# Performance work log

Hardware: AMD Instinct MI355X
Metric: run time of the kernel (lower is better)

The kernel has to match this reference:

```python
import jax, jax.numpy as jnp
import numpy as np

DIM, HEADS, HDIM, B, L = 2048, 16, 128, 2, 2048

def setup_inputs() -> dict:
    key = jax.random.key(0)
    ks = jax.random.split(key, 7)
    s = 1.0 / np.sqrt(DIM)
    return {
        "x": jax.random.normal(ks[0], (B, L, DIM), jnp.float32),
        "rope_emb": jax.random.uniform(ks[1], (L, HDIM), jnp.float32),
        "wq": jax.random.normal(ks[2], (DIM, DIM), jnp.float32) * s,
        "wk": jax.random.normal(ks[3], (DIM, DIM), jnp.float32) * s,
        "wv": jax.random.normal(ks[4], (DIM, DIM), jnp.float32) * s,
        "wo": jax.random.normal(ks[5], (DIM, DIM), jnp.float32) * s,
        "bo": jnp.zeros((DIM,), jnp.float32),
    }

def _rotate_half(x):
    x1, x2 = jnp.split(x, 2, axis=-1)
    return jnp.concatenate((-x2, x1), axis=-1)

def reference(x, rope_emb, wq, wk, wv, wo, bo):
    Bq, Lq, D = x.shape
    # projections; torch Linear: y = x @ W.T, weights here stored as [out,in]
    q = jnp.einsum("bld,ed->ble", x, wq).reshape(Bq, Lq, HEADS, HDIM).transpose(0, 2, 1, 3)
    k = jnp.einsum("bld,ed->ble", x, wk).reshape(Bq, Lq, HEADS, HDIM).transpose(0, 2, 1, 3)
    v = jnp.einsum("bld,ed->ble", x, wv).reshape(Bq, Lq, HEADS, HDIM).transpose(0, 2, 1, 3)
    cos = jnp.cos(rope_emb)[None, None]  # [1,1,L,hd]
    sin = jnp.sin(rope_emb)[None, None]
    q = q * cos + _rotate_half(q) * sin
    k = k * cos + _rotate_half(k) * sin
    scale = HDIM ** -0.5
    attn = jnp.einsum("bhqd,bhkd->bhqk", q, k) * scale
    attn = jax.nn.softmax(attn, axis=-1)
    out = jnp.einsum("bhqk,bhkd->bhqd", attn, v)
    out = out.transpose(0, 2, 1, 3).reshape(Bq, Lq, D)
    return jnp.einsum("bld,ed->ble", out, wo) + bo
```

## Files before the change

### kernel.cpp

```cpp
#include <hip/hip_runtime.h>
#include <hip/hip_bf16.h>
#include <stdint.h>

#define DIMS  2048
#define HEADS 16
#define HD    128
#define BATCH 2
#define SEQ   2048
#define MROWS (BATCH*SEQ)
#define QKVN  (3*DIMS)

using bf16x8 = __attribute__((ext_vector_type(8))) short;
using f32x4  = __attribute__((ext_vector_type(4))) float;
using f32x16 = __attribute__((ext_vector_type(16))) float;
using u16x4  = __attribute__((ext_vector_type(4))) unsigned short;

__device__ __forceinline__ unsigned short f2b(float f){
    __hip_bfloat16 h = __float2bfloat16(f);
    return *reinterpret_cast<unsigned short*>(&h);
}
__device__ __forceinline__ float b2f(unsigned short u){
    __hip_bfloat16 h;
    *reinterpret_cast<unsigned short*>(&h) = u;
    return __bfloat162float(h);
}
__device__ __forceinline__ unsigned int pkbf(float lo, float hi){
    return (unsigned int)f2b(lo) | ((unsigned int)f2b(hi) << 16);
}

__device__ __forceinline__ void glds16(const void* g, void* l){
    __builtin_amdgcn_global_load_lds(
        (const __attribute__((address_space(1))) unsigned int*)g,
        (__attribute__((address_space(3))) unsigned int*)l, 16, 0, 0);
}


__global__ void k_f32bf16(const float* __restrict__ src, unsigned short* __restrict__ dst, int n4){
    int i = blockIdx.x*blockDim.x + threadIdx.x;
    if (i >= n4) return;
    const float4 v = reinterpret_cast<const float4*>(src)[i];
    u16x4 o = { f2b(v.x), f2b(v.y), f2b(v.z), f2b(v.w) };
    *reinterpret_cast<u16x4*>(dst + 4*(size_t)i) = o;
}

__global__ void k_wconv4(const float* __restrict__ w0, const float* __restrict__ w1,
                         const float* __restrict__ w2, const float* __restrict__ w3,
                         unsigned short* __restrict__ d0, unsigned short* __restrict__ d1,
                         unsigned short* __restrict__ d2, unsigned short* __restrict__ d3){
    const int sel = blockIdx.y;
    const float* src = sel==0 ? w0 : sel==1 ? w1 : sel==2 ? w2 : w3;
    unsigned short* dst = sel==0 ? d0 : sel==1 ? d1 : sel==2 ? d2 : d3;
    const int i = blockIdx.x*blockDim.x + threadIdx.x;
    const float4 v = reinterpret_cast<const float4*>(src)[i];
    u16x4 o = { f2b(v.x), f2b(v.y), f2b(v.z), f2b(v.w) };
    *reinterpret_cast<u16x4*>(dst + 4*(size_t)i) = o;
}

__global__ void k_cossin(const float* __restrict__ r, float* __restrict__ c, float* __restrict__ s, int n){
    int i = blockIdx.x*blockDim.x + threadIdx.x;
    if (i >= n) return;
    float v = r[i];
    c[i] = cosf(v);
    s[i] = sinf(v);
}

__global__ void k_rope(unsigned short* __restrict__ qkv,
                       const float* __restrict__ ct, const float* __restrict__ st){
    const int idx = blockIdx.x*blockDim.x + threadIdx.x;
    const int d0 = (idx & 7) << 3;
    const int h  = (idx >> 3) & (HEADS-1);
    const int l  = (idx >> 7) & (SEQ-1);
    const int b  = idx >> 18;

    const float4* cp = reinterpret_cast<const float4*>(ct + l*HD + d0);
    const float4* sp = reinterpret_cast<const float4*>(st + l*HD + d0);
    const float4 cl0 = cp[0],  cl1 = cp[1];
    const float4 sl0 = sp[0],  sl1 = sp[1];
    const float4 cu0 = cp[16], cu1 = cp[17];
    const float4 su0 = sp[16], su1 = sp[17];
    const float cl[8] = {cl0.x,cl0.y,cl0.z,cl0.w, cl1.x,cl1.y,cl1.z,cl1.w};
    const float sl[8] = {sl0.x,sl0.y,sl0.z,sl0.w, sl1.x,sl1.y,sl1.z,sl1.w};
    const float cu[8] = {cu0.x,cu0.y,cu0.z,cu0.w, cu1.x,cu1.y,cu1.z,cu1.w};
    const float su[8] = {su0.x,su0.y,su0.z,su0.w, su1.x,su1.y,su1.z,su1.w};

    unsigned short* base = qkv + (size_t)(b*SEQ + l)*QKVN + h*HD + d0;
    #pragma unroll
    for (int s = 0; s < 2; ++s){
        unsigned short* rp = base + s*DIMS;
        bf16x8 lo = *reinterpret_cast<const bf16x8*>(rp);
        bf16x8 hi = *reinterpret_cast<const bf16x8*>(rp + 64);
        bf16x8 olo, ohi;
        #pragma unroll
        for (int j = 0; j < 8; ++j){
            const float x1 = b2f((unsigned short)lo[j]);
            const float x2 = b2f((unsigned short)hi[j]);
            olo[j] = (short)f2b(x1*cl[j] - x2*sl[j]);
            ohi[j] = (short)f2b(x2*cu[j] + x1*su[j]);
        }
        *reinterpret_cast<bf16x8*>(rp)      = olo;
        *reinterpret_cast<bf16x8*>(rp + 64) = ohi;
    }
}

__global__ void k_vtrans(const unsigned short* __restrict__ qkv, unsigned short* __restrict__ vt){
    __shared__ unsigned short t[64*68];
    const int lt = blockIdx.x;
    const int dt = blockIdx.y;
    const int bh = blockIdx.z;
    const int b = bh >> 4, h = bh & 15;
    const int tid = threadIdx.x;
    const int l0 = lt << 6;
    #pragma unroll
    for (int it = 0; it < 4; ++it){
        const int c = tid + (it<<8);
        const int l = c >> 4;
        const int d4 = (c & 15) << 2;
        const u16x4 v = *reinterpret_cast<const u16x4*>(
            qkv + (size_t)(b*SEQ + l0 + l)*QKVN + 2*DIMS + h*HD + (dt<<6) + d4);
        *reinterpret_cast<u16x4*>(&t[l*68 + d4]) = v;
    }
    __syncthreads();
    #pragma unroll
    for (int it = 0; it < 4; ++it){
        const int c = tid + (it<<8);
        const int d = c >> 4;
        const int l4 = (c & 15) << 2;
        u16x4 o = { t[(l4+0)*68 + d], t[(l4+1)*68 + d], t[(l4+2)*68 + d], t[(l4+3)*68 + d] };
        *reinterpret_cast<u16x4*>(&vt[((size_t)bh*HD + (dt<<6) + d)*SEQ + l0 + l4]) = o;
    }
}


template<int FINAL>
__global__ __launch_bounds__(256) void k_gemm_bt(
    const unsigned short* __restrict__ A, const unsigned short* __restrict__ B,
    void* __restrict__ C, const float* __restrict__ bias, int M, int N, int K)
{
    __shared__ unsigned short lA[128*64];
    __shared__ unsigned short lB[128*64];
    const int tid  = threadIdx.x;
    const int lane = tid & 63;
    const int wave = tid >> 6;

    const int nbx = N >> 7;
    const int nwg = gridDim.x;
    const int cpx = nwg >> 3;
    const int bid = blockIdx.x;
    const int wg  = (bid & 7)*cpx + (bid >> 3);
    const int m0 = (wg / nbx) << 7;
    const int n0 = (wg % nbx) << 7;

    const int wr = (wave >> 1) << 6;
    const int wc = (wave & 1) << 6;

    f32x4 acc[4][4] = {};

    const int srow_base = (wave<<3) + (lane>>3);
    const int schunk = lane & 7;

    for (int k0 = 0; k0 < K; k0 += 64){
        #pragma unroll
        for (int i = 0; i < 4; ++i){
            const int row  = (i<<5) + srow_base;
            const int scol = k0 + ((schunk ^ (row & 7)) << 3);
            glds16(A + (size_t)(m0 + row)*K + scol, &lA[((i<<5) + (wave<<3)) << 6]);
            glds16(B + (size_t)(n0 + row)*K + scol, &lB[((i<<5) + (wave<<3)) << 6]);
        }
        __syncthreads();
        #pragma unroll
        for (int ks = 0; ks < 2; ++ks){
            bf16x8 af[4], bfr[4];
            const int colbase = (ks<<5) + ((lane>>4)<<3);
            #pragma unroll
            for (int mi = 0; mi < 4; ++mi){
                const int row = wr + (mi<<4) + (lane & 15);
                af[mi] = *reinterpret_cast<const bf16x8*>(&lA[(row<<6) + (colbase ^ ((row&7)<<3))]);
            }
            #pragma unroll
            for (int ni = 0; ni < 4; ++ni){
                const int row = wc + (ni<<4) + (lane & 15);
                bfr[ni] = *reinterpret_cast<const bf16x8*>(&lB[(row<<6) + (colbase ^ ((row&7)<<3))]);
            }
            #pragma unroll
            for (int mi = 0; mi < 4; ++mi)
                #pragma unroll
                for (int ni = 0; ni < 4; ++ni)
                    acc[mi][ni] = __builtin_amdgcn_mfma_f32_16x16x32_bf16(af[mi], bfr[ni], acc[mi][ni], 0, 0, 0);
        }
        __syncthreads();
    }

    const int r0 = (lane >> 4) << 2;
    const int cn = lane & 15;
    #pragma unroll
    for (int mi = 0; mi < 4; ++mi)
        #pragma unroll
        for (int r = 0; r < 4; ++r){
            const int gm = m0 + wr + (mi<<4) + r0 + r;
            #pragma unroll
            for (int ni = 0; ni < 4; ++ni){
                const int gn = n0 + wc + (ni<<4) + cn;
                const float v = acc[mi][ni][r];
                if (FINAL)
                    reinterpret_cast<float*>(C)[(size_t)gm*N + gn] = v + bias[gn];
                else
                    reinterpret_cast<unsigned short*>(C)[(size_t)gm*N + gn] = f2b(v);
            }
        }
}


union U8 { unsigned int w[4]; bf16x8 v; };

__global__ __launch_bounds__(256, 2) void k_attn(
    const unsigned short* __restrict__ qkv, const unsigned short* __restrict__ vt,
    unsigned short* __restrict__ aout)
{
    __shared__ unsigned short smem[32768];

    const int tid  = threadIdx.x;
    const int lane = tid & 63;
    const int wave = tid >> 6;
    const int lq   = lane & 31;
    const int hi   = lane >> 5;
    const int bh = blockIdx.y;
    const int b = bh >> 4, h = bh & 15;
    const int q0w = (blockIdx.x << 7) + (wave << 5);

    const unsigned short* Kb = qkv + (size_t)b*SEQ*QKVN + DIMS + h*HD;
    const unsigned short* Vb = vt + (size_t)bh*HD*SEQ;

    bf16x8 qf[8];
    {
        const float qscale = 0.08838834764831845f * 1.4426950408889634f;
        const unsigned short* qp = qkv + (size_t)(b*SEQ + q0w + lq)*QKVN + h*HD + (hi<<3);
        #pragma unroll
        for (int ks = 0; ks < 8; ++ks){
            bf16x8 tv = *reinterpret_cast<const bf16x8*>(qp + (ks<<4));
            #pragma unroll
            for (int j = 0; j < 8; ++j)
                tv[j] = (short)f2b(b2f((unsigned short)tv[j]) * qscale);
            qf[ks] = tv;
        }
    }

    float m_run = -3e38f, l_run = 0.f;
    f32x16 oacc[4] = {};

    #define STAGE(pb, kv0) do { \
        _Pragma("unroll") \
        for (int i = 0; i < 4; ++i){ \
            const int kr = (wave<<4) + (i<<2) + (lane>>4); \
            glds16(Kb + (size_t)((kv0) + kr)*QKVN + (((lane&15) ^ (kr&7))<<3), \
                   &smem[((pb)<<13) + (((wave<<4) + (i<<2))<<7)]); \
            const int dr = (wave<<5) + (i<<3) + (lane>>3); \
            glds16(Vb + (size_t)dr*SEQ + (kv0) + (((lane&7) ^ (dr&7))<<3), \
                   &smem[16384 + ((pb)<<13) + (((wave<<5) + (i<<3))<<6)]); \
        } \
    } while(0)

    int buf = 0;
    STAGE(0, 0);
    __syncthreads();

    for (int t = 0; t < SEQ/64; ++t){
        if (t < SEQ/64 - 1) STAGE(buf^1, (t+1)*64);

        const unsigned short* Kbuf = &smem[buf<<13];
        const unsigned short* Vbuf = &smem[16384 + (buf<<13)];

        f32x16 st0 = {}, st1 = {};
        __builtin_amdgcn_s_setprio(1);
        #pragma unroll
        for (int ks = 0; ks < 8; ++ks){
            const int col = (((ks<<1) + hi) ^ (lq & 7)) << 3;
            bf16x8 k0 = *reinterpret_cast<const bf16x8*>(&Kbuf[(lq<<7) + col]);
            bf16x8 k1 = *reinterpret_cast<const bf16x8*>(&Kbuf[((32+lq)<<7) + col]);
            st0 = __builtin_amdgcn_mfma_f32_32x32x16_bf16(k0, qf[ks], st0, 0, 0, 0);
            st1 = __builtin_amdgcn_mfma_f32_32x32x16_bf16(k1, qf[ks], st1, 0, 0, 0);
        }
        __builtin_amdgcn_s_setprio(0);

        float tmax = st0[0];
        #pragma unroll
        for (int r = 1; r < 16; ++r) tmax = fmaxf(tmax, st0[r]);
        #pragma unroll
        for (int r = 0; r < 16; ++r) tmax = fmaxf(tmax, st1[r]);
        tmax = fmaxf(tmax, __shfl_xor(tmax, 32));

        const bool defer = __all(tmax <= m_run + 8.0f);
        if (!defer){
            const float mnew = fmaxf(m_run, tmax);
            const float al = __builtin_amdgcn_exp2f(m_run - mnew);
            m_run = mnew;
            l_run *= al;
            #pragma unroll
            for (int dt = 0; dt < 4; ++dt) oacc[dt] *= al;
        }
        float tsum = 0.f;
        #pragma unroll
        for (int r = 0; r < 16; ++r){ float p = __builtin_amdgcn_exp2f(st0[r] - m_run); st0[r] = p; tsum += p; }
        #pragma unroll
        for (int r = 0; r < 16; ++r){ float p = __builtin_amdgcn_exp2f(st1[r] - m_run); st1[r] = p; tsum += p; }
        tsum += __shfl_xor(tsum, 32);
        l_run += tsum;

        bf16x8 pf[4];
        #define MAKEPF(dA, dB, SV) do { \
            unsigned int a0 = pkbf(SV[0],SV[1]),  b0 = pkbf(SV[2],SV[3]); \
            unsigned int c0 = pkbf(SV[4],SV[5]),  d0 = pkbf(SV[6],SV[7]); \
            unsigned int a1 = pkbf(SV[8],SV[9]),  b1 = pkbf(SV[10],SV[11]); \
            unsigned int c1 = pkbf(SV[12],SV[13]),d1 = pkbf(SV[14],SV[15]); \
            asm("v_permlane32_swap_b32 %0, %1" : "+v"(a0), "+v"(c0)); \
            asm("v_permlane32_swap_b32 %0, %1" : "+v"(b0), "+v"(d0)); \
            asm("v_permlane32_swap_b32 %0, %1" : "+v"(a1), "+v"(c1)); \
            asm("v_permlane32_swap_b32 %0, %1" : "+v"(b1), "+v"(d1)); \
            U8 u; \
            u.w[0] = a0; u.w[1] = b0; u.w[2] = c0; u.w[3] = d0; dA = u.v; \
            u.w[0] = a1; u.w[1] = b1; u.w[2] = c1; u.w[3] = d1; dB = u.v; \
        } while(0)
        MAKEPF(pf[0], pf[1], st0);
        MAKEPF(pf[2], pf[3], st1);
        #undef MAKEPF

        __builtin_amdgcn_s_setprio(1);
        #pragma unroll
        for (int dt = 0; dt < 4; ++dt){
            const int rowv = (dt<<5) + lq;
            #pragma unroll
            for (int f = 0; f < 4; ++f){
                const int col = (((f<<1) + hi) ^ (lq & 7)) << 3;
                bf16x8 vf = *reinterpret_cast<const bf16x8*>(&Vbuf[(rowv<<6) + col]);
                oacc[dt] = __builtin_amdgcn_mfma_f32_32x32x16_bf16(vf, pf[f], oacc[dt], 0, 0, 0);
            }
        }
        __builtin_amdgcn_s_setprio(0);

        __syncthreads();
        buf ^= 1;
    }
    #undef STAGE

    const float rl = 1.0f / l_run;
    unsigned short* oL = smem + wave*(32*132);
    #pragma unroll
    for (int dt = 0; dt < 4; ++dt)
        #pragma unroll
        for (int g = 0; g < 4; ++g){
            u16x4 w = { f2b(oacc[dt][g*4+0]*rl), f2b(oacc[dt][g*4+1]*rl),
                        f2b(oacc[dt][g*4+2]*rl), f2b(oacc[dt][g*4+3]*rl) };
            *reinterpret_cast<u16x4*>(&oL[lq*132 + (dt<<5) + (hi<<2) + (g<<3)]) = w;
        }
    #pragma unroll
    for (int i = 0; i < 16; ++i){
        const int q = (i<<1) + hi;
        u16x4 w = *reinterpret_cast<const u16x4*>(&oL[q*132 + (lq<<2)]);
        *reinterpret_cast<u16x4*>(&aout[(size_t)(b*SEQ + q0w + q)*DIMS + h*HD + (lq<<2)]) = w;
    }
}


extern "C" void kernel_launch(void* const* d_in, const int* in_sizes, int n_in,
                              void* d_out, int out_size, void* d_ws, size_t ws_size,
                              hipStream_t stream)
{
    const float* x    = (const float*)d_in[0];
    const float* rope = (const float*)d_in[1];
    const float* wq   = (const float*)d_in[2];
    const float* wk   = (const float*)d_in[3];
    const float* wv   = (const float*)d_in[4];
    const float* wo   = (const float*)d_in[5];
    const float* bo   = (const float*)d_in[6];
    float* out = (float*)d_out;

    char* ws = (char*)d_ws;
    unsigned short* x_bf   = (unsigned short*)(ws + 0);
    unsigned short* wqkv   = (unsigned short*)(ws + 16777216);
    unsigned short* wo_bf  = (unsigned short*)(ws + 41943040);
    float*          cos_t  = (float*)(ws + 50331648);
    float*          sin_t  = (float*)(ws + 51380224);
    unsigned short* qkv    = (unsigned short*)(ws + 52428800);
    unsigned short* vt     = (unsigned short*)(ws + 16777216);
    unsigned short* a_out  = (unsigned short*)(ws + 0);

    k_f32bf16<<<8192, 256, 0, stream>>>(x, x_bf, 2097152);
    k_wconv4<<<dim3(4096,4), 256, 0, stream>>>(wq, wk, wv, wo,
                                               wqkv, wqkv + 4194304, wqkv + 8388608, wo_bf);
    k_cossin <<<1024, 256, 0, stream>>>(rope, cos_t, sin_t, SEQ*HD);

    k_gemm_bt<0><<<(MROWS/128)*(QKVN/128), 256, 0, stream>>>(x_bf, wqkv, qkv, nullptr, MROWS, QKVN, DIMS);

    k_rope<<<2048, 256, 0, stream>>>(qkv, cos_t, sin_t);

    k_vtrans<<<dim3(SEQ/64, HD/64, BATCH*HEADS), 256, 0, stream>>>(qkv, vt);

    k_attn<<<dim3(SEQ/128, BATCH*HEADS), 256, 0, stream>>>(qkv, vt, a_out);

    k_gemm_bt<1><<<(MROWS/128)*(DIMS/128), 256, 0, stream>>>(a_out, wo_bf, out, bo, MROWS, DIMS, DIMS);
}
```

Measured before the change: 287.5 us.

## Merge prep kernels, fuse K-rope with V transpose, apply Q-rope inside attention

Folds the x/weight bf16 conversions and the cos/sin table into one launch. K-rope and the V transpose now share a single kernel, which removes two launches and the separate Q-rope pass over global memory. Q rotary embedding is applied in registers while Q fragments are loaded in the attention kernel, combined with the softmax scale. The trade-off is extra cos/sin table loads and arithmetic in attention setup, plus a larger branchy prep grid.

```diff
diff --git a/kernel.cpp b/kernel.cpp
--- a/kernel.cpp
+++ b/kernel.cpp
@@ -35,58 +35,60 @@
 }
 
 
-__global__ void k_f32bf16(const float* __restrict__ src, unsigned short* __restrict__ dst, int n4){
-    int i = blockIdx.x*blockDim.x + threadIdx.x;
-    if (i >= n4) return;
+__global__ void k_prep(const float* __restrict__ x,
+                       const float* __restrict__ w0, const float* __restrict__ w1,
+                       const float* __restrict__ w2, const float* __restrict__ w3,
+                       const float* __restrict__ rope,
+                       unsigned short* __restrict__ x_bf,
+                       unsigned short* __restrict__ d0, unsigned short* __restrict__ d1,
+                       unsigned short* __restrict__ d2, unsigned short* __restrict__ d3,
+                       float* __restrict__ ct, float* __restrict__ st){
+    const int y = blockIdx.y;
+    if (y == 6){
+        const int i = blockIdx.x*blockDim.x + threadIdx.x;
+        if (i >= SEQ*HD) return;
+        const float v = rope[i];
+        ct[i] = cosf(v);
+        st[i] = sinf(v);
+        return;
+    }
+    const float* src;
+    unsigned short* dst;
+    size_t off = 0;
+    if      (y == 0){ src = w0; dst = d0; }
+    else if (y == 1){ src = w1; dst = d1; }
+    else if (y == 2){ src = w2; dst = d2; }
+    else if (y == 3){ src = w3; dst = d3; }
+    else            { src = x;  dst = x_bf; off = (size_t)(y - 4) * 1048576; }
+    const size_t i = off + blockIdx.x*blockDim.x + threadIdx.x;
     const float4 v = reinterpret_cast<const float4*>(src)[i];
     u16x4 o = { f2b(v.x), f2b(v.y), f2b(v.z), f2b(v.w) };
-    *reinterpret_cast<u16x4*>(dst + 4*(size_t)i) = o;
-}
-
-__global__ void k_wconv4(const float* __restrict__ w0, const float* __restrict__ w1,
-                         const float* __restrict__ w2, const float* __restrict__ w3,
-                         unsigned short* __restrict__ d0, unsigned short* __restrict__ d1,
-                         unsigned short* __restrict__ d2, unsigned short* __restrict__ d3){
-    const int sel = blockIdx.y;
-    const float* src = sel==0 ? w0 : sel==1 ? w1 : sel==2 ? w2 : w3;
-    unsigned short* dst = sel==0 ? d0 : sel==1 ? d1 : sel==2 ? d2 : d3;
-    const int i = blockIdx.x*blockDim.x + threadIdx.x;
-    const float4 v = reinterpret_cast<const float4*>(src)[i];
-    u16x4 o = { f2b(v.x), f2b(v.y), f2b(v.z), f2b(v.w) };
-    *reinterpret_cast<u16x4*>(dst + 4*(size_t)i) = o;
-}
-
-__global__ void k_cossin(const float* __restrict__ r, float* __restrict__ c, float* __restrict__ s, int n){
-    int i = blockIdx.x*blockDim.x + threadIdx.x;
-    if (i >= n) return;
-    float v = r[i];
-    c[i] = cosf(v);
-    s[i] = sinf(v);
-}
-
-__global__ void k_rope(unsigned short* __restrict__ qkv,
-                       const float* __restrict__ ct, const float* __restrict__ st){
-    const int idx = blockIdx.x*blockDim.x + threadIdx.x;
-    const int d0 = (idx & 7) << 3;
-    const int h  = (idx >> 3) & (HEADS-1);
-    const int l  = (idx >> 7) & (SEQ-1);
-    const int b  = idx >> 18;
-
-    const float4* cp = reinterpret_cast<const float4*>(ct + l*HD + d0);
-    const float4* sp = reinterpret_cast<const float4*>(st + l*HD + d0);
-    const float4 cl0 = cp[0],  cl1 = cp[1];
-    const float4 sl0 = sp[0],  sl1 = sp[1];
-    const float4 cu0 = cp[16], cu1 = cp[17];
-    const float4 su0 = sp[16], su1 = sp[17];
-    const float cl[8] = {cl0.x,cl0.y,cl0.z,cl0.w, cl1.x,cl1.y,cl1.z,cl1.w};
-    const float sl[8] = {sl0.x,sl0.y,sl0.z,sl0.w, sl1.x,sl1.y,sl1.z,sl1.w};
-    const float cu[8] = {cu0.x,cu0.y,cu0.z,cu0.w, cu1.x,cu1.y,cu1.z,cu1.w};
-    const float su[8] = {su0.x,su0.y,su0.z,su0.w, su1.x,su1.y,su1.z,su1.w};
-
-    unsigned short* base = qkv + (size_t)(b*SEQ + l)*QKVN + h*HD + d0;
-    #pragma unroll
-    for (int s = 0; s < 2; ++s){
-        unsigned short* rp = base + s*DIMS;
+    *reinterpret_cast<u16x4*>(dst + 4*i) = o;
+}
+
+
+__global__ void k_kropevt(unsigned short* __restrict__ qkv,
+                          const float* __restrict__ ct, const float* __restrict__ st,
+                          unsigned short* __restrict__ vt){
+    __shared__ unsigned short t[64*68];
+    const int bid = blockIdx.x;
+    if (bid < 2048){
+        const int idx = bid*blockDim.x + threadIdx.x;
+        const int d0 = (idx & 7) << 3;
+        const int h  = (idx >> 3) & (HEADS-1);
+        const int l  = (idx >> 7) & (SEQ-1);
+        const int b  = idx >> 18;
+        const float4* cp = reinterpret_cast<const float4*>(ct + l*HD + d0);
+        const float4* sp = reinterpret_cast<const float4*>(st + l*HD + d0);
+        const float4 cl0 = cp[0],  cl1 = cp[1];
+        const float4 sl0 = sp[0],  sl1 = sp[1];
+        const float4 cu0 = cp[16], cu1 = cp[17];
+        const float4 su0 = sp[16], su1 = sp[17];
+        const float cl[8] = {cl0.x,cl0.y,cl0.z,cl0.w, cl1.x,cl1.y,cl1.z,cl1.w};
+        const float sl[8] = {sl0.x,sl0.y,sl0.z,sl0.w, sl1.x,sl1.y,sl1.z,sl1.w};
+        const float cu[8] = {cu0.x,cu0.y,cu0.z,cu0.w, cu1.x,cu1.y,cu1.z,cu1.w};
+        const float su[8] = {su0.x,su0.y,su0.z,su0.w, su1.x,su1.y,su1.z,su1.w};
+        unsigned short* rp = qkv + (size_t)(b*SEQ + l)*QKVN + DIMS + h*HD + d0;
         bf16x8 lo = *reinterpret_cast<const bf16x8*>(rp);
         bf16x8 hi = *reinterpret_cast<const bf16x8*>(rp + 64);
         bf16x8 olo, ohi;
@@ -99,14 +101,12 @@
         }
         *reinterpret_cast<bf16x8*>(rp)      = olo;
         *reinterpret_cast<bf16x8*>(rp + 64) = ohi;
-    }
-}
-
-__global__ void k_vtrans(const unsigned short* __restrict__ qkv, unsigned short* __restrict__ vt){
-    __shared__ unsigned short t[64*68];
-    const int lt = blockIdx.x;
-    const int dt = blockIdx.y;
-    const int bh = blockIdx.z;
+        return;
+    }
+    const int bid2 = bid - 2048;
+    const int lt = bid2 & 31;
+    const int dt = (bid2 >> 5) & 1;
+    const int bh = bid2 >> 6;
     const int b = bh >> 4, h = bh & 15;
     const int tid = threadIdx.x;
     const int l0 = lt << 6;
@@ -214,6 +214,7 @@
 
 __global__ __launch_bounds__(256, 2) void k_attn(
     const unsigned short* __restrict__ qkv, const unsigned short* __restrict__ vt,
+    const float* __restrict__ ct, const float* __restrict__ st,
     unsigned short* __restrict__ aout)
 {
     __shared__ unsigned short smem[32768];
@@ -233,14 +234,33 @@
     bf16x8 qf[8];
     {
         const float qscale = 0.08838834764831845f * 1.4426950408889634f;
-        const unsigned short* qp = qkv + (size_t)(b*SEQ + q0w + lq)*QKVN + h*HD + (hi<<3);
-        #pragma unroll
-        for (int ks = 0; ks < 8; ++ks){
-            bf16x8 tv = *reinterpret_cast<const bf16x8*>(qp + (ks<<4));
-            #pragma unroll
-            for (int j = 0; j < 8; ++j)
-                tv[j] = (short)f2b(b2f((unsigned short)tv[j]) * qscale);
-            qf[ks] = tv;
+        const int l = q0w + lq;
+        const unsigned short* qp = qkv + (size_t)(b*SEQ + l)*QKVN + h*HD + (hi<<3);
+        #pragma unroll
+        for (int ks = 0; ks < 8; ++ks)
+            qf[ks] = *reinterpret_cast<const bf16x8*>(qp + (ks<<4));
+        #pragma unroll
+        for (int ks = 0; ks < 4; ++ks){
+            const int d0 = (ks<<4) + (hi<<3);
+            const float4 c0 = *reinterpret_cast<const float4*>(ct + l*HD + d0);
+            const float4 c1 = *reinterpret_cast<const float4*>(ct + l*HD + d0 + 4);
+            const float4 s0 = *reinterpret_cast<const float4*>(st + l*HD + d0);
+            const float4 s1 = *reinterpret_cast<const float4*>(st + l*HD + d0 + 4);
+            const float4 C0 = *reinterpret_cast<const float4*>(ct + l*HD + d0 + 64);
+            const float4 C1 = *reinterpret_cast<const float4*>(ct + l*HD + d0 + 68);
+            const float4 S0 = *reinterpret_cast<const float4*>(st + l*HD + d0 + 64);
+            const float4 S1 = *reinterpret_cast<const float4*>(st + l*HD + d0 + 68);
+            const float cl[8] = {c0.x,c0.y,c0.z,c0.w, c1.x,c1.y,c1.z,c1.w};
+            const float sl[8] = {s0.x,s0.y,s0.z,s0.w, s1.x,s1.y,s1.z,s1.w};
+            const float cu[8] = {C0.x,C0.y,C0.z,C0.w, C1.x,C1.y,C1.z,C1.w};
+            const float su[8] = {S0.x,S0.y,S0.z,S0.w, S1.x,S1.y,S1.z,S1.w};
+            #pragma unroll
+            for (int j = 0; j < 8; ++j){
+                const float x1 = b2f((unsigned short)qf[ks][j]);
+                const float x2 = b2f((unsigned short)qf[ks+4][j]);
+                qf[ks][j]   = (short)f2b((x1*cl[j] - x2*sl[j]) * qscale);
+                qf[ks+4][j] = (short)f2b((x2*cu[j] + x1*su[j]) * qscale);
+            }
         }
     }
 
@@ -383,18 +403,15 @@
     unsigned short* vt     = (unsigned short*)(ws + 16777216);
     unsigned short* a_out  = (unsigned short*)(ws + 0);
 
-    k_f32bf16<<<8192, 256, 0, stream>>>(x, x_bf, 2097152);
-    k_wconv4<<<dim3(4096,4), 256, 0, stream>>>(wq, wk, wv, wo,
-                                               wqkv, wqkv + 4194304, wqkv + 8388608, wo_bf);
-    k_cossin <<<1024, 256, 0, stream>>>(rope, cos_t, sin_t, SEQ*HD);
+    k_prep<<<dim3(4096, 7), 256, 0, stream>>>(x, wq, wk, wv, wo, rope,
+                                              x_bf, wqkv, wqkv + 4194304, wqkv + 8388608, wo_bf,
+                                              cos_t, sin_t);
 
     k_gemm_bt<0><<<(MROWS/128)*(QKVN/128), 256, 0, stream>>>(x_bf, wqkv, qkv, nullptr, MROWS, QKVN, DIMS);
 
-    k_rope<<<2048, 256, 0, stream>>>(qkv, cos_t, sin_t);
-
-    k_vtrans<<<dim3(SEQ/64, HD/64, BATCH*HEADS), 256, 0, stream>>>(qkv, vt);
-
-    k_attn<<<dim3(SEQ/128, BATCH*HEADS), 256, 0, stream>>>(qkv, vt, a_out);
+    k_kropevt<<<4096, 256, 0, stream>>>(qkv, cos_t, sin_t, vt);
+
+    k_attn<<<dim3(SEQ/128, BATCH*HEADS), 256, 0, stream>>>(qkv, vt, cos_t, sin_t, a_out);
 
     k_gemm_bt<1><<<(MROWS/128)*(DIMS/128), 256, 0, stream>>>(a_out, wo_bf, out, bo, MROWS, DIMS, DIMS);
 }
```

Result: no change. 285.7 us, median of 2 (-0.6%).
